# Kernel optimization log

Measured on AMD Instinct MI355X. Metric: run time of the kernel, lower is better.

## Reference

```python
import jax, jax.numpy as jnp
import numpy as np

N = 100000      # n_nodes
D = 64          # in_features (= out_features)
H = 4           # attention heads
DK = D // H     # per-head dim
E = 1600000     # num edges (avg degree 16)
STEP = 0.25     # ODE euler step size
NSTEPS = 4      # integrate t in [0, 1]
ALPHA = 0.2     # LeakyReLU negative slope


def setup_inputs() -> dict:
    key = jax.random.key(0)
    k1, k2, k3, k4 = jax.random.split(key, 4)
    x = jax.random.normal(k1, (N, D), dtype=jnp.float32)
    edge_index = jax.random.randint(k2, (2, E), 0, N, dtype=jnp.int32)
    edge_weight = jax.random.uniform(k3, (E,), dtype=jnp.float32)
    # HamAgg.weight: init.eye_ -> identity [D, D]
    W = jnp.eye(D, dtype=jnp.float32)
    # HAM_GATConv.a: xavier_normal_ on shape (2*d_k, 1, 1), gain=1.414
    a = jax.random.normal(k4, (2 * DK,), dtype=jnp.float32) * (1.414 * np.sqrt(2.0 / (2 * DK + 1)))
    return {"x": x, "edge_index": edge_index, "edge_weight": edge_weight, "W": W, "a": a}


def reference(x, edge_index, edge_weight, W, a):
    # ---- Hamiltonian ODE block (args.vt == 'fc', odemap 'h1extend') ----
    # xt = hstack([x, x @ W.T]); euler-integrate canonical Hamiltonian flow
    # dq/dt = p, dp/dt = -q over t in [0,1] with step 0.25; keep first D dims.
    q = x
    p = x @ W.T
    for _ in range(NSTEPS):
        q, p = q + STEP * p, p - STEP * q
    xt = q  # out_x = out[..., :D]

    row, col = edge_index[0], edge_index[1]

    # ---- HAM_GATConv attention (W_x = x @ I = x) ----
    # h[n, head, k] = xt[n, head*DK + k]
    h = xt.reshape(N, H, DK)
    a_src, a_dst = a[:DK], a[DK:]
    s_src = h @ a_src   # [N, H] per-node source contribution
    s_dst = h @ a_dst   # [N, H] per-node dest contribution
    score = jax.nn.leaky_relu(s_src[row] + s_dst[col], ALPHA)  # [E, H]

    # segment softmax grouped by destination (edge[1])
    seg_max = jax.ops.segment_max(score, col, num_segments=N)  # [N, H]
    seg_max = jnp.where(jnp.isfinite(seg_max), seg_max, 0.0)
    e = jnp.exp(score - seg_max[col])
    denom = jax.ops.segment_sum(e, col, num_segments=N)
    att = e / (denom[col] + 1e-16)  # [E, H]

    # ---- mean over heads of per-head spmm == single spmm with mean attention ----
    # spmm: out[row[e]] += att[e] * xt[col[e]]
    w = att.mean(axis=1)  # [E]
    out = jax.ops.segment_sum(w[:, None] * xt[col], row, num_segments=N)  # [N, D]
    return out
```

## Files before the change

kernel.cpp:

```cpp
#include <hip/hip_runtime.h>
#include <hip/hip_bf16.h>


#define LRELU(v) ((v) > 0.0f ? (v) : 0.2f * (v))

#define EC 4096
#define BSC 64
#define BSR 128
#define SLOTS 4

typedef __attribute__((ext_vector_type(8))) short bf16x8;
typedef __attribute__((ext_vector_type(4))) float f32x4;

__device__ __forceinline__ float bf16_to_f32(unsigned short u) {
    return __uint_as_float((unsigned int)u << 16);
}
__device__ __forceinline__ float bflo(unsigned int u) {
    return __uint_as_float(u << 16);
}
__device__ __forceinline__ float bfhi(unsigned int u) {
    return __uint_as_float(u & 0xFFFF0000u);
}
__device__ __forceinline__ unsigned short f32_to_bf16(float f) {
    __hip_bfloat16 h = __float2bfloat16(f);
    return *reinterpret_cast<unsigned short*>(&h);
}

__global__ __launch_bounds__(256) void k_geff(const float* __restrict__ W,
                                              const float* __restrict__ a,
                                              unsigned short* __restrict__ geff16,
                                              float c1, float c2) {
    int t = threadIdx.x;
    int k = t & 63, h = t >> 6;
    float ssrc = 0.0f, sdst = 0.0f;
#pragma unroll
    for (int d = 0; d < 16; ++d) {
        float w = W[(h * 16 + d) * 64 + k];
        ssrc += w * a[d];
        sdst += w * a[16 + d];
    }
    float gsrc = c2 * ssrc, gdst = c2 * sdst;
    if ((k >> 4) == h) {
        gsrc += c1 * a[k & 15];
        gdst += c1 * a[16 + (k & 15)];
    }
    unsigned short sh = f32_to_bf16(gsrc);
    unsigned short sl = f32_to_bf16(gsrc - bf16_to_f32(sh));
    unsigned short dh = f32_to_bf16(gdst);
    unsigned short dl = f32_to_bf16(gdst - bf16_to_f32(dh));
    geff16[h * 64 + k] = sh;
    geff16[(4 + h) * 64 + k] = dh;
    geff16[(8 + h) * 64 + k] = sl;
    geff16[(12 + h) * 64 + k] = dl;
}

__global__ __launch_bounds__(256) void k_node(const float* __restrict__ x,
                                              const float* __restrict__ W,
                                              const unsigned short* __restrict__ geff16,
                                              unsigned short* __restrict__ xt16,
                                              float* __restrict__ s_src,
                                              float* __restrict__ s_dst,
                                              int n, float c1, float c2) {
    int wave = threadIdx.x >> 6;
    int lane = threadIdx.x & 63;
    int nb = blockIdx.x * 64 + wave * 16;
    if (nb >= n) return;
    int colg = lane & 15;
    int grp = lane >> 4;
    int k0 = grp << 3;

    bf16x8 wf[4][2];
#pragma unroll
    for (int ct = 0; ct < 4; ++ct) {
#pragma unroll
        for (int ks = 0; ks < 2; ++ks) {
            const float* wr = W + (size_t)(ct * 16 + colg) * 64 + k0 + ks * 32;
            float4 w0 = *(const float4*)(wr);
            float4 w1 = *(const float4*)(wr + 4);
            bf16x8 f;
            f[0] = (short)f32_to_bf16(w0.x); f[1] = (short)f32_to_bf16(w0.y);
            f[2] = (short)f32_to_bf16(w0.z); f[3] = (short)f32_to_bf16(w0.w);
            f[4] = (short)f32_to_bf16(w1.x); f[5] = (short)f32_to_bf16(w1.y);
            f[6] = (short)f32_to_bf16(w1.z); f[7] = (short)f32_to_bf16(w1.w);
            wf[ct][ks] = f;
        }
    }
    bf16x8 gf[2];
#pragma unroll
    for (int ks = 0; ks < 2; ++ks)
        gf[ks] = *(const bf16x8*)(geff16 + colg * 64 + k0 + ks * 32);

    int arow = nb + colg;
    if (arow >= n) arow = n - 1;
    const float* xr = x + (size_t)arow * 64 + k0;
    bf16x8 af[2];
#pragma unroll
    for (int ks = 0; ks < 2; ++ks) {
        float4 x0 = *(const float4*)(xr + ks * 32);
        float4 x1 = *(const float4*)(xr + ks * 32 + 4);
        bf16x8 f;
        f[0] = (short)f32_to_bf16(x0.x); f[1] = (short)f32_to_bf16(x0.y);
        f[2] = (short)f32_to_bf16(x0.z); f[3] = (short)f32_to_bf16(x0.w);
        f[4] = (short)f32_to_bf16(x1.x); f[5] = (short)f32_to_bf16(x1.y);
        f[6] = (short)f32_to_bf16(x1.z); f[7] = (short)f32_to_bf16(x1.w);
        af[ks] = f;
    }

    f32x4 acc[5];
#pragma unroll
    for (int i = 0; i < 5; ++i) acc[i] = (f32x4){0.f, 0.f, 0.f, 0.f};
#pragma unroll
    for (int ct = 0; ct < 4; ++ct) {
        acc[ct] = __builtin_amdgcn_mfma_f32_16x16x32_bf16(af[0], wf[ct][0], acc[ct], 0, 0, 0);
        acc[ct] = __builtin_amdgcn_mfma_f32_16x16x32_bf16(af[1], wf[ct][1], acc[ct], 0, 0, 0);
    }
    acc[4] = __builtin_amdgcn_mfma_f32_16x16x32_bf16(af[0], gf[0], acc[4], 0, 0, 0);
    acc[4] = __builtin_amdgcn_mfma_f32_16x16x32_bf16(af[1], gf[1], acc[4], 0, 0, 0);

#pragma unroll
    for (int ct = 0; ct < 4; ++ct) {
        int col = ct * 16 + colg;
#pragma unroll
        for (int rr = 0; rr < 4; ++rr) {
            int node = nb + grp * 4 + rr;
            if (node < n) {
                float xv = x[(size_t)node * 64 + col];
                float xtv = c1 * xv + c2 * acc[ct][rr];
                xt16[(size_t)node * 64 + col] = f32_to_bf16(xtv);
            }
        }
    }
#pragma unroll
    for (int rr = 0; rr < 4; ++rr) {
        float v = acc[4][rr];
        float tot = v + __shfl_xor(v, 8, 64);
        int node = nb + grp * 4 + rr;
        if (node < n) {
            if (colg < 4) s_src[node * 4 + colg] = tot;
            else if (colg < 8) s_dst[node * 4 + (colg - 4)] = tot;
        }
    }
}

__global__ __launch_bounds__(256) void k_hist(const int* __restrict__ row,
                                              const int* __restrict__ col,
                                              int* __restrict__ Hr,
                                              int* __restrict__ Hc,
                                              int e, int nblk, int nbr, int nbc) {
    __shared__ int hr[1024];
    __shared__ int hc[2048];
    int t = threadIdx.x;
    for (int i = t; i < 1024; i += 256) hr[i] = 0;
    for (int i = t; i < 2048; i += 256) hc[i] = 0;
    __syncthreads();
    int base = blockIdx.x * EC;
#pragma unroll
    for (int j = 0; j < EC / 256; ++j) {
        int i = base + t + j * 256;
        if (i < e) {
            atomicAdd(&hr[row[i] >> 7], 1);
            atomicAdd(&hc[col[i] >> 6], 1);
        }
    }
    __syncthreads();
    for (int b = t; b < nbr; b += 256) Hr[(size_t)b * nblk + blockIdx.x] = hr[b];
    for (int b = t; b < nbc; b += 256) Hc[(size_t)b * nblk + blockIdx.x] = hc[b];
}

__global__ __launch_bounds__(256) void k_scanH2(int* __restrict__ Hr,
                                                int* __restrict__ Hc,
                                                int* __restrict__ BtotR,
                                                int* __restrict__ BtotC,
                                                int nblk, int nbr) {
    __shared__ int vals[512];
    __shared__ int part[256];
    int t = threadIdx.x;
    int bb = blockIdx.x;
    int* Hb;
    int* Btot;
    if (bb < nbr) {
        Hb = Hr + (size_t)bb * nblk;
        Btot = BtotR + bb;
    } else {
        Hb = Hc + (size_t)(bb - nbr) * nblk;
        Btot = BtotC + (bb - nbr);
    }
    for (int i = t; i < nblk; i += 256) vals[i] = Hb[i];
    __syncthreads();
    int c0 = t * 2;
    int s = 0;
#pragma unroll
    for (int j = 0; j < 2; ++j)
        if (c0 + j < nblk) s += vals[c0 + j];
    part[t] = s;
    __syncthreads();
    for (int d = 1; d < 256; d <<= 1) {
        int add = (t >= d) ? part[t - d] : 0;
        __syncthreads();
        part[t] += add;
        __syncthreads();
    }
    int run = part[t] - s;
#pragma unroll
    for (int j = 0; j < 2; ++j) {
        int i = c0 + j;
        if (i < nblk) {
            int v = vals[i];
            Hb[i] = run;
            run += v;
        }
    }
    if (t == 255) *Btot = part[255];
}

__global__ __launch_bounds__(256) void k_base2(const int* __restrict__ BtotR,
                                               int* __restrict__ BbR, int nbr,
                                               const int* __restrict__ BtotC,
                                               int* __restrict__ BbC, int nbc) {
    const int* Btot = (blockIdx.x == 0) ? BtotR : BtotC;
    int* Bbase = (blockIdx.x == 0) ? BbR : BbC;
    int nb = (blockIdx.x == 0) ? nbr : nbc;
    __shared__ int part[256];
    __shared__ int carry;
    int t = threadIdx.x;
    if (t == 0) carry = 0;
    __syncthreads();
    for (int base = 0; base < nb; base += 256) {
        int i = base + t;
        int v = (i < nb) ? Btot[i] : 0;
        part[t] = v;
        __syncthreads();
        for (int d = 1; d < 256; d <<= 1) {
            int add = (t >= d) ? part[t - d] : 0;
            __syncthreads();
            part[t] += add;
            __syncthreads();
        }
        if (i < nb) Bbase[i] = carry + part[t] - v;
        __syncthreads();
        if (t == 0) carry += part[255];
        __syncthreads();
    }
    if (t == 0) Bbase[nb] = carry;
}

__global__ __launch_bounds__(256) void k_scatter_dual(
    const int* __restrict__ row, const int* __restrict__ col,
    const int* __restrict__ Hr, const int* __restrict__ Hc,
    const int* __restrict__ BbR, const int* __restrict__ BbC,
    int* __restrict__ ebr, int* __restrict__ ebc,
    int e, int nblk, int nbr, int nbc) {
    __shared__ int curr[1024];
    __shared__ int curc[2048];
    int t = threadIdx.x;
    int blk = blockIdx.x;
    for (int b = t; b < nbr; b += 256) curr[b] = BbR[b] + Hr[(size_t)b * nblk + blk];
    for (int b = t; b < nbc; b += 256) curc[b] = BbC[b] + Hc[(size_t)b * nblk + blk];
    __syncthreads();
    int base = blk * EC;
#pragma unroll
    for (int j = 0; j < EC / 256; ++j) {
        int i = base + t + j * 256;
        if (i < e) {
            int r = row[i], c = col[i];
            int pr = atomicAdd(&curr[r >> 7], 1);
            ebr[pr] = (c << 7) | (r & 127);
            int pc = atomicAdd(&curc[c >> 6], 1);
            ebc[pc] = (r << 6) | (c & 63);
        }
    }
}

__global__ __launch_bounds__(256) void k_denom_b(const int* __restrict__ ebc,
                                                 const int* __restrict__ BbC,
                                                 const float* __restrict__ s_src,
                                                 const float* __restrict__ s_dst,
                                                 float* __restrict__ rden, int n) {
    __shared__ float acc[BSC * 4];
    __shared__ float sd[BSC * 4];
    int t = threadIdx.x;
    int b = blockIdx.x;
    int cbase = b << 6;
    if (t < BSC * 4) {
        acc[t] = 0.0f;
        int c4 = cbase * 4 + t;
        sd[t] = (c4 < n * 4) ? s_dst[c4] : 0.0f;
    }
    __syncthreads();
    int start = BbC[b], end = BbC[b + 1];
    for (int i = start + t; i < end; i += 256) {
        int p = ebc[i];
        int r = p >> 6, cl = p & 63;
        float4 ss = *(const float4*)(s_src + (size_t)r * 4);
        atomicAdd(&acc[cl * 4 + 0], __expf(LRELU(ss.x + sd[cl * 4 + 0])));
        atomicAdd(&acc[cl * 4 + 1], __expf(LRELU(ss.y + sd[cl * 4 + 1])));
        atomicAdd(&acc[cl * 4 + 2], __expf(LRELU(ss.z + sd[cl * 4 + 2])));
        atomicAdd(&acc[cl * 4 + 3], __expf(LRELU(ss.w + sd[cl * 4 + 3])));
    }
    __syncthreads();
    if (t < BSC * 4) {
        int c4 = cbase * 4 + t;
        if (c4 < n * 4) rden[c4] = 1.0f / (acc[t] + 1e-16f);
    }
}

__global__ __launch_bounds__(256) void k_sort2(const int* __restrict__ ebr,
                                               const int* __restrict__ BbR,
                                               const float* __restrict__ s_src,
                                               const float* __restrict__ s_dst,
                                               const float* __restrict__ rden,
                                               int* __restrict__ rowptr,
                                               int2* __restrict__ cwp,
                                               int n, int e) {
    __shared__ int cnt[BSR];
    __shared__ int pfx[BSR];
    __shared__ int cur[BSR];
    __shared__ float ssh[BSR * 4];
    int t = threadIdx.x;
    int b = blockIdx.x;
    int rbase = b << 7;
    if (t < BSR) cnt[t] = 0;
    for (int i = t; i < BSR * 4; i += 256) {
        int g = rbase * 4 + i;
        ssh[i] = (g < n * 4) ? s_src[g] : 0.0f;
    }
    __syncthreads();
    int start = BbR[b], end = BbR[b + 1];
    for (int i = start + t; i < end; i += 256)
        atomicAdd(&cnt[ebr[i] & 127], 1);
    __syncthreads();
    if (t < BSR) pfx[t] = cnt[t];
    __syncthreads();
    for (int d = 1; d < BSR; d <<= 1) {
        int v = (t < BSR && t >= d) ? pfx[t - d] : 0;
        __syncthreads();
        if (t < BSR) pfx[t] += v;
        __syncthreads();
    }
    if (t < BSR) {
        int excl = start + pfx[t] - cnt[t];
        cur[t] = excl;
        int r = rbase + t;
        if (r < n) rowptr[r] = excl;
    }
    if (b == 0 && t == 0) rowptr[n] = e;
    __syncthreads();
    for (int i = start + t; i < end; i += 256) {
        int p = ebr[i];
        int rl = p & 127, c = p >> 7;
        float4 sd = *(const float4*)(s_dst + (size_t)c * 4);
        float4 rd = *(const float4*)(rden + (size_t)c * 4);
        float wv = __expf(LRELU(ssh[rl * 4 + 0] + sd.x)) * rd.x +
                   __expf(LRELU(ssh[rl * 4 + 1] + sd.y)) * rd.y +
                   __expf(LRELU(ssh[rl * 4 + 2] + sd.z)) * rd.z +
                   __expf(LRELU(ssh[rl * 4 + 3] + sd.w)) * rd.w;
        int pos = atomicAdd(&cur[rl], 1);
        cwp[pos] = make_int2(c << 6, __float_as_int(0.25f * wv));
    }
}

__global__ __launch_bounds__(256) void k_aggr(const int* __restrict__ rowptr,
                                              const int2* __restrict__ cwp,
                                              const unsigned short* __restrict__ xt16,
                                              float* __restrict__ out, int n, int e) {
    int r = blockIdx.x * 4 + (threadIdx.x >> 6);
    if (r >= n) return;
    int lane = threadIdx.x & 63;
    int g = lane >> 3;
    unsigned le = (lane & 7) << 3;
    int start = rowptr[r], end = rowptr[r + 1];
    float acc[8];
#pragma unroll
    for (int j = 0; j < 8; ++j) acc[j] = 0.0f;
    for (int base = start; base < end; base += SLOTS * 8) {
        int m = end - base;
        if (m > SLOTS * 8) m = SLOTS * 8;
        int nk = (m + 7) >> 3;
        uint4 u[SLOTS];
        float wv[SLOTS];
#pragma unroll
        for (int k = 0; k < SLOTS; ++k) {
            if (k < nk) {
                int idx = base + k * 8 + g;
                int idc = idx < e ? idx : e - 1;
                int2 cw = cwp[idc];
                wv[k] = (idx < end) ? __int_as_float(cw.y) : 0.0f;
                u[k] = *(const uint4*)(xt16 + ((unsigned)cw.x + le));
            }
        }
#pragma unroll
        for (int k = 0; k < SLOTS; ++k) {
            if (k < nk) {
                acc[0] = fmaf(wv[k], bflo(u[k].x), acc[0]);
                acc[1] = fmaf(wv[k], bfhi(u[k].x), acc[1]);
                acc[2] = fmaf(wv[k], bflo(u[k].y), acc[2]);
                acc[3] = fmaf(wv[k], bfhi(u[k].y), acc[3]);
                acc[4] = fmaf(wv[k], bflo(u[k].z), acc[4]);
                acc[5] = fmaf(wv[k], bfhi(u[k].z), acc[5]);
                acc[6] = fmaf(wv[k], bflo(u[k].w), acc[6]);
                acc[7] = fmaf(wv[k], bfhi(u[k].w), acc[7]);
            }
        }
    }
#pragma unroll
    for (int off = 8; off <= 32; off <<= 1) {
#pragma unroll
        for (int j = 0; j < 8; ++j) acc[j] += __shfl_xor(acc[j], off, 64);
    }
    if (lane < 8) {
        float4 a0 = {acc[0], acc[1], acc[2], acc[3]};
        float4 a1 = {acc[4], acc[5], acc[6], acc[7]};
        *(float4*)(out + (size_t)r * 64 + le) = a0;
        *(float4*)(out + (size_t)r * 64 + le + 4) = a1;
    }
}

extern "C" void kernel_launch(void* const* d_in, const int* in_sizes, int n_in,
                              void* d_out, int out_size, void* d_ws, size_t ws_size,
                              hipStream_t stream) {
    const float* x = (const float*)d_in[0];
    const int* ei = (const int*)d_in[1];
    const float* W = (const float*)d_in[3];
    const float* a = (const float*)d_in[4];
    int n = in_sizes[0] / 64;
    int e = in_sizes[1] / 2;
    const int* row = ei;
    const int* col = ei + e;
    float* out = (float*)d_out;

    int nblk = (e + EC - 1) / EC;
    int nbr = (n + BSR - 1) / BSR;
    int nbc = (n + BSC - 1) / BSC;

    size_t o = 0;
    auto take = [&](size_t cnt) {
        size_t p = o;
        o += (cnt + 3) & ~(size_t)3;
        return p;
    };
    int* wsi = (int*)d_ws;
    unsigned short* xt16 = (unsigned short*)(wsi + take((size_t)n * 32));
    float* s_src = (float*)(wsi + take((size_t)n * 4));
    float* s_dst = (float*)(wsi + take((size_t)n * 4));
    float* rden = (float*)(wsi + take((size_t)n * 4));
    unsigned short* geff16 = (unsigned short*)(wsi + take(512));
    int* Hr = wsi + take((size_t)nbr * nblk);
    int* Hc = wsi + take((size_t)nbc * nblk);
    int* BtotR = wsi + take(nbr);
    int* BbR = wsi + take(nbr + 1);
    int* BtotC = wsi + take(nbc);
    int* BbC = wsi + take(nbc + 1);
    int* ebr = wsi + take(e);
    int* cwbuf = wsi + take((size_t)2 * e);
    int* ebc = cwbuf;
    int2* cwp = (int2*)cwbuf;
    int* rowptr = wsi + take(n + 1);

    float aq = 1.f, bq = 0.f, ap = 0.f, bp = 1.f;
    for (int i = 0; i < 4; ++i) {
        float naq = aq + 0.25f * ap, nbq = bq + 0.25f * bp;
        float nap = ap - 0.25f * aq, nbp = bp - 0.25f * bq;
        aq = naq; bq = nbq; ap = nap; bp = nbp;
    }

    k_geff<<<1, 256, 0, stream>>>(W, a, geff16, aq, bq);
    k_node<<<(n + 63) / 64, 256, 0, stream>>>(x, W, geff16, xt16, s_src, s_dst,
                                              n, aq, bq);
    k_hist<<<nblk, 256, 0, stream>>>(row, col, Hr, Hc, e, nblk, nbr, nbc);
    k_scanH2<<<nbr + nbc, 256, 0, stream>>>(Hr, Hc, BtotR, BtotC, nblk, nbr);
    k_base2<<<2, 256, 0, stream>>>(BtotR, BbR, nbr, BtotC, BbC, nbc);
    k_scatter_dual<<<nblk, 256, 0, stream>>>(row, col, Hr, Hc, BbR, BbC,
                                             ebr, ebc, e, nblk, nbr, nbc);
    k_denom_b<<<nbc, 256, 0, stream>>>(ebc, BbC, s_src, s_dst, rden, n);
    k_sort2<<<nbr, 256, 0, stream>>>(ebr, BbR, s_src, s_dst, rden,
                                     rowptr, cwp, n, e);
    k_aggr<<<(n + 3) / 4, 256, 0, stream>>>(rowptr, cwp, xt16, out, n, e);
}
```

Baseline: 314.5 us.

## Halve edge chunk and row bucket sizes, interleave dst score with reciprocal denom

The edge chunk per block drops to 2048 and the row bucket width to 64 nodes. This doubles the number of blocks in the histogram, scatter and sort kernels to raise parallelism, and it widens the per-bucket scan to four entries per thread. The denominator kernel now writes s_dst and the reciprocal denominator side by side into one 8-float record per node. This lets the sort kernel fetch both with adjacent loads instead of gathering from two separate arrays. Trade-offs are larger histogram matrices, more scan work per bucket, and more atomics contention per bucket in shared memory.

After: 324.8 us. 1.03x slower.

```diff
diff --git a/kernel.cpp b/kernel.cpp
--- a/kernel.cpp
+++ b/kernel.cpp
@@ -4,9 +4,9 @@
 
 #define LRELU(v) ((v) > 0.0f ? (v) : 0.2f * (v))
 
-#define EC 4096
+#define EC 2048
 #define BSC 64
-#define BSR 128
+#define BSR 64
 #define SLOTS 4
 
 typedef __attribute__((ext_vector_type(8))) short bf16x8;
@@ -147,18 +147,17 @@
                                               int* __restrict__ Hr,
                                               int* __restrict__ Hc,
                                               int e, int nblk, int nbr, int nbc) {
-    __shared__ int hr[1024];
+    __shared__ int hr[2048];
     __shared__ int hc[2048];
     int t = threadIdx.x;
-    for (int i = t; i < 1024; i += 256) hr[i] = 0;
-    for (int i = t; i < 2048; i += 256) hc[i] = 0;
+    for (int i = t; i < 2048; i += 256) { hr[i] = 0; hc[i] = 0; }
     __syncthreads();
     int base = blockIdx.x * EC;
 #pragma unroll
     for (int j = 0; j < EC / 256; ++j) {
         int i = base + t + j * 256;
         if (i < e) {
-            atomicAdd(&hr[row[i] >> 7], 1);
+            atomicAdd(&hr[row[i] >> 6], 1);
             atomicAdd(&hc[col[i] >> 6], 1);
         }
     }
@@ -172,7 +171,7 @@
                                                 int* __restrict__ BtotR,
                                                 int* __restrict__ BtotC,
                                                 int nblk, int nbr) {
-    __shared__ int vals[512];
+    __shared__ int vals[1024];
     __shared__ int part[256];
     int t = threadIdx.x;
     int bb = blockIdx.x;
@@ -187,10 +186,10 @@
     }
     for (int i = t; i < nblk; i += 256) vals[i] = Hb[i];
     __syncthreads();
-    int c0 = t * 2;
+    int c0 = t * 4;
     int s = 0;
 #pragma unroll
-    for (int j = 0; j < 2; ++j)
+    for (int j = 0; j < 4; ++j)
         if (c0 + j < nblk) s += vals[c0 + j];
     part[t] = s;
     __syncthreads();
@@ -202,7 +201,7 @@
     }
     int run = part[t] - s;
 #pragma unroll
-    for (int j = 0; j < 2; ++j) {
+    for (int j = 0; j < 4; ++j) {
         int i = c0 + j;
         if (i < nblk) {
             int v = vals[i];
@@ -250,7 +249,7 @@
     const int* __restrict__ BbR, const int* __restrict__ BbC,
     int* __restrict__ ebr, int* __restrict__ ebc,
     int e, int nblk, int nbr, int nbc) {
-    __shared__ int curr[1024];
+    __shared__ int curr[2048];
     __shared__ int curc[2048];
     int t = threadIdx.x;
     int blk = blockIdx.x;
@@ -263,8 +262,8 @@
         int i = base + t + j * 256;
         if (i < e) {
             int r = row[i], c = col[i];
-            int pr = atomicAdd(&curr[r >> 7], 1);
-            ebr[pr] = (c << 7) | (r & 127);
+            int pr = atomicAdd(&curr[r >> 6], 1);
+            ebr[pr] = (c << 6) | (r & 63);
             int pc = atomicAdd(&curc[c >> 6], 1);
             ebc[pc] = (r << 6) | (c & 63);
         }
@@ -275,7 +274,7 @@
                                                  const int* __restrict__ BbC,
                                                  const float* __restrict__ s_src,
                                                  const float* __restrict__ s_dst,
-                                                 float* __restrict__ rden, int n) {
+                                                 float* __restrict__ sdr, int n) {
     __shared__ float acc[BSC * 4];
     __shared__ float sd[BSC * 4];
     int t = threadIdx.x;
@@ -299,16 +298,19 @@
     }
     __syncthreads();
     if (t < BSC * 4) {
-        int c4 = cbase * 4 + t;
-        if (c4 < n * 4) rden[c4] = 1.0f / (acc[t] + 1e-16f);
+        int c = cbase + (t >> 2);
+        if (c < n) {
+            int h = t & 3;
+            sdr[(size_t)c * 8 + h] = sd[t];
+            sdr[(size_t)c * 8 + 4 + h] = 1.0f / (acc[t] + 1e-16f);
+        }
     }
 }
 
 __global__ __launch_bounds__(256) void k_sort2(const int* __restrict__ ebr,
                                                const int* __restrict__ BbR,
                                                const float* __restrict__ s_src,
-                                               const float* __restrict__ s_dst,
-                                               const float* __restrict__ rden,
+                                               const float* __restrict__ sdr,
                                                int* __restrict__ rowptr,
                                                int2* __restrict__ cwp,
                                                int n, int e) {
@@ -318,16 +320,16 @@
     __shared__ float ssh[BSR * 4];
     int t = threadIdx.x;
     int b = blockIdx.x;
-    int rbase = b << 7;
+    int rbase = b << 6;
     if (t < BSR) cnt[t] = 0;
-    for (int i = t; i < BSR * 4; i += 256) {
-        int g = rbase * 4 + i;
-        ssh[i] = (g < n * 4) ? s_src[g] : 0.0f;
+    if (t < BSR * 4) {
+        int g = rbase * 4 + t;
+        ssh[t] = (g < n * 4) ? s_src[g] : 0.0f;
     }
     __syncthreads();
     int start = BbR[b], end = BbR[b + 1];
     for (int i = start + t; i < end; i += 256)
-        atomicAdd(&cnt[ebr[i] & 127], 1);
+        atomicAdd(&cnt[ebr[i] & 63], 1);
     __syncthreads();
     if (t < BSR) pfx[t] = cnt[t];
     __syncthreads();
@@ -347,9 +349,9 @@
     __syncthreads();
     for (int i = start + t; i < end; i += 256) {
         int p = ebr[i];
-        int rl = p & 127, c = p >> 7;
-        float4 sd = *(const float4*)(s_dst + (size_t)c * 4);
-        float4 rd = *(const float4*)(rden + (size_t)c * 4);
+        int rl = p & 63, c = p >> 6;
+        float4 sd = *(const float4*)(sdr + (size_t)c * 8);
+        float4 rd = *(const float4*)(sdr + (size_t)c * 8 + 4);
         float wv = __expf(LRELU(ssh[rl * 4 + 0] + sd.x)) * rd.x +
                    __expf(LRELU(ssh[rl * 4 + 1] + sd.y)) * rd.y +
                    __expf(LRELU(ssh[rl * 4 + 2] + sd.z)) * rd.z +
@@ -442,7 +444,7 @@
     unsigned short* xt16 = (unsigned short*)(wsi + take((size_t)n * 32));
     float* s_src = (float*)(wsi + take((size_t)n * 4));
     float* s_dst = (float*)(wsi + take((size_t)n * 4));
-    float* rden = (float*)(wsi + take((size_t)n * 4));
+    float* sdr = (float*)(wsi + take((size_t)n * 8));
     unsigned short* geff16 = (unsigned short*)(wsi + take(512));
     int* Hr = wsi + take((size_t)nbr * nblk);
     int* Hc = wsi + take((size_t)nbc * nblk);
@@ -471,8 +473,7 @@
     k_base2<<<2, 256, 0, stream>>>(BtotR, BbR, nbr, BtotC, BbC, nbc);
     k_scatter_dual<<<nblk, 256, 0, stream>>>(row, col, Hr, Hc, BbR, BbC,
                                              ebr, ebc, e, nblk, nbr, nbc);
-    k_denom_b<<<nbc, 256, 0, stream>>>(ebc, BbC, s_src, s_dst, rden, n);
-    k_sort2<<<nbr, 256, 0, stream>>>(ebr, BbR, s_src, s_dst, rden,
-                                     rowptr, cwp, n, e);
+    k_denom_b<<<nbc, 256, 0, stream>>>(ebc, BbC, s_src, s_dst, sdr, n);
+    k_sort2<<<nbr, 256, 0, stream>>>(ebr, BbR, s_src, sdr, rowptr, cwp, n, e);
     k_aggr<<<(n + 3) / 4, 256, 0, stream>>>(rowptr, cwp, xt16, out, n, e);
 }
```
